# Kernel tuning notes

Measured on AMD Instinct MI355X. Metric: run time of the kernel, lower is better.

Reference implementation:

```python
import jax, jax.numpy as jnp
import numpy as np

COMMITMENT_COST = 0.25


def setup_inputs() -> dict:
    key = jax.random.key(0)
    k1, k2 = jax.random.split(key)
    inputs = jax.random.normal(k1, (16, 4096, 256), dtype=jnp.float32)
    codewords = jax.random.normal(k2, (1024, 256), dtype=jnp.float32)
    return {"inputs": inputs, "codewords": codewords}


def reference(inputs, codewords):
    # inputs: (*, D), codewords: (K, D)
    D = codewords.shape[-1]
    flat = inputs.reshape(-1, D)  # (N, D)
    x_sq = jnp.sum(flat * flat, axis=-1, keepdims=True)            # (N, 1)
    c_sq = jnp.sum(codewords * codewords, axis=-1)                 # (K,)
    distances = x_sq - 2.0 * (flat @ codewords.T) + c_sq           # (N, K)
    encoding_indices = jnp.argmin(distances, axis=1)               # (N,)
    quantized = codewords[encoding_indices].reshape(inputs.shape)  # (*, D)
    # Straight-through estimator
    quantized_st = inputs + jax.lax.stop_gradient(quantized - inputs)
    quantizing_loss = jnp.mean((quantized_st - jax.lax.stop_gradient(inputs)) ** 2)
    commitment_loss = jnp.mean((jax.lax.stop_gradient(quantized_st) - inputs) ** 2)
    loss = quantizing_loss + COMMITMENT_COST * commitment_loss
    return quantized_st, encoding_indices.reshape(inputs.shape[:-1]), loss
```

## Files before the change

kernel.cpp:

```cpp
#include <hip/hip_runtime.h>
#include <math.h>

typedef _Float16 v8h __attribute__((ext_vector_type(8)));
typedef float v4f __attribute__((ext_vector_type(4)));

constexpr int D      = 256;
constexpr int KS     = 8;
constexpr int TILE_B = 8192;
constexpr int TPW    = 2;
constexpr int WIN_B  = 16384;
constexpr int NWIN   = 32;
#define GUARD 1.0f

__global__ void vq_prep(const float* __restrict__ cw, unsigned short* __restrict__ img) {
    int gid = blockIdx.x * 256 + threadIdx.x;
    int t  = gid >> 9;
    int r  = gid & 511;
    int ks = r >> 6;
    int l  = r & 63;
    int cand = t * 16 + (l & 15);
    int k0   = ks * 32 + (l >> 4) * 8;
    const float* src = cw + (size_t)cand * D + k0;
    float4 t0 = *(const float4*)(src);
    float4 t1 = *(const float4*)(src + 4);
    v8h h;
    h[0] = (_Float16)t0.x; h[1] = (_Float16)t0.y;
    h[2] = (_Float16)t0.z; h[3] = (_Float16)t0.w;
    h[4] = (_Float16)t1.x; h[5] = (_Float16)t1.y;
    h[6] = (_Float16)t1.z; h[7] = (_Float16)t1.w;
    *(v8h*)((char*)img + (size_t)gid * 16) = h;
}

__global__ void vq_csq(const float* __restrict__ cw, float* __restrict__ csq) {
    int k = blockIdx.x * blockDim.x + threadIdx.x;
    const float4* p = reinterpret_cast<const float4*>(cw + (size_t)k * D);
    float s = 0.f;
    #pragma unroll 8
    for (int i = 0; i < D / 4; ++i) {
        float4 v = p[i];
        s += v.x * v.x; s += v.y * v.y; s += v.z * v.z; s += v.w * v.w;
    }
    csq[k] = s;
}

__launch_bounds__(256, 2)
__global__ void vq_main(const float* __restrict__ inp,
                        const float* __restrict__ cw,
                        const unsigned short* __restrict__ img,
                        const float* __restrict__ csq,
                        float* __restrict__ outq,
                        float* __restrict__ outi,
                        float* __restrict__ bsum) {
    __shared__ __align__(16) char smem[3][WIN_B];
    __shared__ float s_cq[1024];
    __shared__ int4  s_pack[128];
    __shared__ float s_xsq[128];
    __shared__ int   s_win[128];
    __shared__ float s_l[4];

    const int tid  = threadIdx.x;
    const int lane = tid & 63;
    const int w    = tid >> 6;
    const int lr   = lane & 15;
    const int q    = lane >> 4;
    const int base = blockIdx.x * 128 + w * 32;

#define VQ_STAGE(WIN, BUF)                                                           \
    {                                                                                \
        const char* srct = (const char*)img + (size_t)(WIN) * WIN_B;                 \
        _Pragma("unroll")                                                            \
        for (int i = 0; i < 4; ++i) {                                                \
            int off = i * 4096 + w * 1024;                                           \
            __builtin_amdgcn_global_load_lds(                                        \
                (const __attribute__((address_space(1))) unsigned int*)(srct + off + lane * 16), \
                (__attribute__((address_space(3))) unsigned int*)(&smem[BUF][off]),  \
                16, 0, 0);                                                           \
        }                                                                            \
    }

    VQ_STAGE(0, 0)
    VQ_STAGE(1, 1)

    {
        float4 cv4 = ((const float4*)csq)[tid];
        s_cq[tid * 4 + 0] = cv4.x + 4096.f;
        s_cq[tid * 4 + 1] = cv4.y + 4096.f;
        s_cq[tid * 4 + 2] = cv4.z + 4096.f;
        s_cq[tid * 4 + 3] = cv4.w + 4096.f;
    }

    v8h a2[2][8];
    #pragma unroll
    for (int m = 0; m < 2; ++m) {
        const float* rp = inp + (size_t)(base + m * 16 + lr) * D + q * 8;
        float sq = 0.f;
        #pragma unroll
        for (int ks = 0; ks < KS; ++ks) {
            float4 t0 = *(const float4*)(rp + ks * 32);
            float4 t1 = *(const float4*)(rp + ks * 32 + 4);
            sq = fmaf(t0.x, t0.x, sq); sq = fmaf(t0.y, t0.y, sq);
            sq = fmaf(t0.z, t0.z, sq); sq = fmaf(t0.w, t0.w, sq);
            sq = fmaf(t1.x, t1.x, sq); sq = fmaf(t1.y, t1.y, sq);
            sq = fmaf(t1.z, t1.z, sq); sq = fmaf(t1.w, t1.w, sq);
            v8h h;
            h[0] = (_Float16)(-2.f * t0.x); h[1] = (_Float16)(-2.f * t0.y);
            h[2] = (_Float16)(-2.f * t0.z); h[3] = (_Float16)(-2.f * t0.w);
            h[4] = (_Float16)(-2.f * t1.x); h[5] = (_Float16)(-2.f * t1.y);
            h[6] = (_Float16)(-2.f * t1.z); h[7] = (_Float16)(-2.f * t1.w);
            a2[m][ks] = h;
        }
        sq += __shfl_xor(sq, 16);
        sq += __shfl_xor(sq, 32);
        if (q == 0) s_xsq[w * 32 + m * 16 + lr] = sq;
    }

    const float BIGF = __uint_as_float(0x7F000000u);
    float v1[2][4], v2[2][4];
    #pragma unroll
    for (int m = 0; m < 2; ++m)
        #pragma unroll
        for (int r = 0; r < 4; ++r) { v1[m][r] = BIGF; v2[m][r] = BIGF; }

    __syncthreads();

#define VQ_COMPUTE(BUF, WIN)                                                         \
    {                                                                                \
        float cq0 = s_cq[(2 * (WIN)) * 16 + lr];                                     \
        float cq1 = s_cq[(2 * (WIN) + 1) * 16 + lr];                                 \
        v4f a00 = {cq0, cq0, cq0, cq0}; v4f a01 = a00;                               \
        v4f a10 = {cq1, cq1, cq1, cq1}; v4f a11 = a10;                               \
        const char* bb = smem[BUF];                                                  \
        __builtin_amdgcn_s_setprio(1);                                               \
        _Pragma("unroll")                                                            \
        for (int ks = 0; ks < KS; ++ks) {                                            \
            v8h b0 = *(const v8h*)(bb + ks * 1024 + lane * 16);                      \
            v8h b1 = *(const v8h*)(bb + TILE_B + ks * 1024 + lane * 16);             \
            a00 = __builtin_amdgcn_mfma_f32_16x16x32_f16(a2[0][ks], b0, a00, 0, 0, 0); \
            a10 = __builtin_amdgcn_mfma_f32_16x16x32_f16(a2[0][ks], b1, a10, 0, 0, 0); \
            a01 = __builtin_amdgcn_mfma_f32_16x16x32_f16(a2[1][ks], b0, a01, 0, 0, 0); \
            a11 = __builtin_amdgcn_mfma_f32_16x16x32_f16(a2[1][ks], b1, a11, 0, 0, 0); \
        }                                                                            \
        __builtin_amdgcn_s_setprio(0);                                               \
        unsigned idx0 = (unsigned)((2 * (WIN)) * 16) | (unsigned)lr;                 \
        unsigned idx1 = (unsigned)((2 * (WIN) + 1) * 16) | (unsigned)lr;             \
        _Pragma("unroll")                                                            \
        for (int r = 0; r < 4; ++r) {                                                \
            float f;                                                                 \
            f = __uint_as_float(((__float_as_uint(a00[r]) + 0x200u) & 0xFFFFFC00u) | idx0); \
            { float mx = fmaxf(v1[0][r], f); v2[0][r] = fminf(v2[0][r], mx); v1[0][r] = fminf(v1[0][r], f); } \
            f = __uint_as_float(((__float_as_uint(a01[r]) + 0x200u) & 0xFFFFFC00u) | idx0); \
            { float mx = fmaxf(v1[1][r], f); v2[1][r] = fminf(v2[1][r], mx); v1[1][r] = fminf(v1[1][r], f); } \
            f = __uint_as_float(((__float_as_uint(a10[r]) + 0x200u) & 0xFFFFFC00u) | idx1); \
            { float mx = fmaxf(v1[0][r], f); v2[0][r] = fminf(v2[0][r], mx); v1[0][r] = fminf(v1[0][r], f); } \
            f = __uint_as_float(((__float_as_uint(a11[r]) + 0x200u) & 0xFFFFFC00u) | idx1); \
            { float mx = fmaxf(v1[1][r], f); v2[1][r] = fminf(v2[1][r], mx); v1[1][r] = fminf(v1[1][r], f); } \
        }                                                                            \
    }

    int cm = 0;
    int st = 2;
    for (int win = 0; win < NWIN - 1; ++win) {
        asm volatile("s_waitcnt vmcnt(4)" ::: "memory");
        __builtin_amdgcn_s_barrier();
        __builtin_amdgcn_sched_barrier(0);
        if (win + 2 < NWIN) VQ_STAGE(win + 2, st)
        __builtin_amdgcn_sched_barrier(0);
        VQ_COMPUTE(cm, win)
        cm = (cm == 2) ? 0 : cm + 1;
        st = (st == 2) ? 0 : st + 1;
    }
    asm volatile("s_waitcnt vmcnt(0)" ::: "memory");
    __builtin_amdgcn_s_barrier();
    __builtin_amdgcn_sched_barrier(0);
    VQ_COMPUTE(cm, NWIN - 1)
#undef VQ_COMPUTE
#undef VQ_STAGE

    #pragma unroll
    for (int m = 0; m < 2; ++m)
        #pragma unroll
        for (int r = 0; r < 4; ++r) {
            float L0 = v1[m][r], L1 = v2[m][r], L2 = BIGF, L3 = BIGF;
            #pragma unroll
            for (int off = 8; off; off >>= 1) {
                float P0 = __shfl_xor(L0, off, 16);
                float P1 = __shfl_xor(L1, off, 16);
                float P2 = __shfl_xor(L2, off, 16);
                float P3 = __shfl_xor(L3, off, 16);
                float M0 = fminf(L0, P3), M1 = fminf(L1, P2);
                float M2 = fminf(L2, P1), M3 = fminf(L3, P0);
                float a0 = fminf(M0, M2), c0 = fmaxf(M0, M2);
                float b0 = fminf(M1, M3), d0 = fmaxf(M1, M3);
                L0 = fminf(a0, b0); L1 = fmaxf(a0, b0);
                L2 = fminf(c0, d0); L3 = fmaxf(c0, d0);
            }
            if (lr == 0) {
                int rloc = m * 16 + q * 4 + r;
                s_pack[w * 32 + rloc] = make_int4(
                    (int)__float_as_uint(L0), (int)__float_as_uint(L1),
                    (int)__float_as_uint(L2), (int)__float_as_uint(L3));
            }
        }

    const int c = lane & 3;
    float lacc = 0.f;
    #pragma unroll
    for (int h = 0; h < 2; ++h) {
        int rloc = h * 16 + (lane >> 2);
        int grow = base + rloc;
        int4 pk = s_pack[w * 32 + rloc];
        float L0 = __uint_as_float((unsigned)pk.x);
        float L1 = __uint_as_float((unsigned)pk.y);
        float L2 = __uint_as_float((unsigned)pk.z);
        float L3 = __uint_as_float((unsigned)pk.w);
        float xq = s_xsq[w * 32 + rloc];

        int   bi;
        float bd;
        bool rescue = (L1 - L0) < GUARD;
        if (rescue) {
            float Lc = (c == 0) ? L0 : (c == 1) ? L1 : (c == 2) ? L2 : L3;
            int cd = (int)(__float_as_uint(Lc) & 1023u);
            const float4* xp = (const float4*)(inp + (size_t)grow * D);
            const float4* cp = (const float4*)(cw + (size_t)cd * D);
            float dot = 0.f, xsq = 0.f;
            #pragma unroll 8
            for (int i = 0; i < D / 4; ++i) {
                float4 xv = xp[i];
                float4 cv = cp[i];
                xsq = fmaf(xv.x, xv.x, xsq);
                xsq = fmaf(xv.y, xv.y, xsq);
                xsq = fmaf(xv.z, xv.z, xsq);
                xsq = fmaf(xv.w, xv.w, xsq);
                dot = fmaf(xv.x, cv.x, dot);
                dot = fmaf(xv.y, cv.y, dot);
                dot = fmaf(xv.z, cv.z, dot);
                dot = fmaf(xv.w, cv.w, dot);
            }
            float m2 = dot + dot;
            float t  = xsq - m2;
            float e  = t + csq[cd];
            bd = e; bi = cd;
            #pragma unroll
            for (int off = 1; off <= 2; off <<= 1) {
                float ev = __shfl_xor(bd, off, 4);
                int   iv = __shfl_xor(bi, off, 4);
                bool  tk = (ev < bd) || (ev == bd && iv < bi);
                bd = tk ? ev : bd;
                bi = tk ? iv : bi;
            }
        } else {
            bi = (int)(__float_as_uint(L0) & 1023u);
            bd = (L0 - 4096.f) + xq;
        }

        if (c == 0) { s_win[w * 32 + rloc] = bi; lacc += bd; }
    }

    #pragma unroll 4
    for (int rr = 0; rr < 32; ++rr) {
        int bw = s_win[w * 32 + rr];
        float4 cv = *(const float4*)(cw + (size_t)bw * D + lane * 4);
        *(float4*)(outq + (size_t)(base + rr) * D + lane * 4) = cv;
        if (lane == 0) outi[base + rr] = (float)bw;
    }

    #pragma unroll
    for (int off = 32; off; off >>= 1) lacc += __shfl_xor(lacc, off);
    if (lane == 0) s_l[w] = lacc;
    __syncthreads();
    if (tid == 0) bsum[blockIdx.x] = s_l[0] + s_l[1] + s_l[2] + s_l[3];
}

__global__ void vq_finalize(const float* __restrict__ bsum, float* __restrict__ out_loss,
                            int nb, float scale) {
    __shared__ float s[4];
    int tid = threadIdx.x;
    float v = 0.f;
    for (int i = tid; i < nb; i += 256) v += bsum[i];
    #pragma unroll
    for (int off = 32; off; off >>= 1) v += __shfl_down(v, off, 64);
    if ((tid & 63) == 0) s[tid >> 6] = v;
    __syncthreads();
    if (tid == 0) out_loss[0] = (s[0] + s[1] + s[2] + s[3]) * scale;
}

extern "C" void kernel_launch(void* const* d_in, const int* in_sizes, int n_in,
                              void* d_out, int out_size, void* d_ws, size_t ws_size,
                              hipStream_t stream) {
    const float* inp = (const float*)d_in[0];
    const float* cw  = (const float*)d_in[1];
    float* out = (float*)d_out;
    const int N = in_sizes[0] / D;
    const int K = in_sizes[1] / D;

    char* ws = (char*)d_ws;
    unsigned short* img = (unsigned short*)ws;
    float* csq  = (float*)(ws + (size_t)K * D * 2);
    float* bsum = csq + K;

    float* outq = out;
    float* outi = out + (size_t)N * D;
    float* outl = outi + N;

    vq_prep<<<dim3((K * 32) / 256), dim3(256), 0, stream>>>(cw, img);
    vq_csq<<<dim3(K / 256), dim3(256), 0, stream>>>(cw, csq);

    vq_main<<<dim3(N / 128), dim3(256), 0, stream>>>(inp, cw, img, csq,
                                                     outq, outi, bsum);
    vq_finalize<<<dim3(1), dim3(256), 0, stream>>>(bsum, outl, N / 128,
                                                   1.25f / ((float)N * (float)D));
}
```

Measured before the change: 91.10 us.

## Split codeword windows across wave pairs with 64 rows per wave

Waves are paired: each wave now holds 64 input rows (four 16-row A fragments) and computes only half of each staged codeword window, so each wave reads one B fragment per k-step and reuses it across four MFMAs instead of two. The codeword image layout is permuted in the prep kernel so each window's two halves are contiguous, and per-row top-4 candidates from the two halves are merged through shared memory after an added block barrier. This cuts LDS reads per MFMA but doubles the A-fragment registers per wave, which may reduce occupancy, and duplicates the input-row loads across wave pairs.

```diff
diff --git a/kernel.cpp b/kernel.cpp
--- a/kernel.cpp
+++ b/kernel.cpp
@@ -6,8 +6,7 @@
 
 constexpr int D      = 256;
 constexpr int KS     = 8;
-constexpr int TILE_B = 8192;
-constexpr int TPW    = 2;
+constexpr int HALF_B = 8192;
 constexpr int WIN_B  = 16384;
 constexpr int NWIN   = 32;
 #define GUARD 1.0f
@@ -28,7 +27,8 @@
     h[2] = (_Float16)t0.z; h[3] = (_Float16)t0.w;
     h[4] = (_Float16)t1.x; h[5] = (_Float16)t1.y;
     h[6] = (_Float16)t1.z; h[7] = (_Float16)t1.w;
-    *(v8h*)((char*)img + (size_t)gid * 16) = h;
+    size_t dst = (size_t)(t & 31) * WIN_B + (size_t)(t >> 5) * HALF_B + ks * 1024 + l * 16;
+    *(v8h*)((char*)img + dst) = h;
 }
 
 __global__ void vq_csq(const float* __restrict__ cw, float* __restrict__ csq) {
@@ -53,7 +53,7 @@
                         float* __restrict__ bsum) {
     __shared__ __align__(16) char smem[3][WIN_B];
     __shared__ float s_cq[1024];
-    __shared__ int4  s_pack[128];
+    __shared__ int4  s_pk[2][128];
     __shared__ float s_xsq[128];
     __shared__ int   s_win[128];
     __shared__ float s_l[4];
@@ -61,9 +61,11 @@
     const int tid  = threadIdx.x;
     const int lane = tid & 63;
     const int w    = tid >> 6;
+    const int hh   = w & 1;
+    const int g    = w >> 1;
     const int lr   = lane & 15;
     const int q    = lane >> 4;
-    const int base = blockIdx.x * 128 + w * 32;
+    const int rbase = blockIdx.x * 128 + g * 64;
 
 #define VQ_STAGE(WIN, BUF)                                                           \
     {                                                                                \
@@ -89,10 +91,10 @@
         s_cq[tid * 4 + 3] = cv4.w + 4096.f;
     }
 
-    v8h a2[2][8];
-    #pragma unroll
-    for (int m = 0; m < 2; ++m) {
-        const float* rp = inp + (size_t)(base + m * 16 + lr) * D + q * 8;
+    v8h a2[4][8];
+    #pragma unroll
+    for (int m = 0; m < 4; ++m) {
+        const float* rp = inp + (size_t)(rbase + m * 16 + lr) * D + q * 8;
         float sq = 0.f;
         #pragma unroll
         for (int ks = 0; ks < KS; ++ks) {
@@ -111,13 +113,13 @@
         }
         sq += __shfl_xor(sq, 16);
         sq += __shfl_xor(sq, 32);
-        if (q == 0) s_xsq[w * 32 + m * 16 + lr] = sq;
+        if (hh == 0 && q == 0) s_xsq[g * 64 + m * 16 + lr] = sq;
     }
 
     const float BIGF = __uint_as_float(0x7F000000u);
-    float v1[2][4], v2[2][4];
-    #pragma unroll
-    for (int m = 0; m < 2; ++m)
+    float v1[4][4], v2[4][4];
+    #pragma unroll
+    for (int m = 0; m < 4; ++m)
         #pragma unroll
         for (int r = 0; r < 4; ++r) { v1[m][r] = BIGF; v2[m][r] = BIGF; }
 
@@ -125,40 +127,36 @@
 
 #define VQ_COMPUTE(BUF, WIN)                                                         \
     {                                                                                \
-        float cq0 = s_cq[(2 * (WIN)) * 16 + lr];                                     \
-        float cq1 = s_cq[(2 * (WIN) + 1) * 16 + lr];                                 \
-        v4f a00 = {cq0, cq0, cq0, cq0}; v4f a01 = a00;                               \
-        v4f a10 = {cq1, cq1, cq1, cq1}; v4f a11 = a10;                               \
-        const char* bb = smem[BUF];                                                  \
+        const int tile = (WIN) + (hh << 5);                                          \
+        float cq = s_cq[tile * 16 + lr];                                             \
+        v4f a0 = {cq, cq, cq, cq}; v4f a1 = a0; v4f aa2 = a0; v4f a3 = a0;           \
+        const char* bb = smem[BUF] + hh * HALF_B;                                    \
         __builtin_amdgcn_s_setprio(1);                                               \
         _Pragma("unroll")                                                            \
         for (int ks = 0; ks < KS; ++ks) {                                            \
-            v8h b0 = *(const v8h*)(bb + ks * 1024 + lane * 16);                      \
-            v8h b1 = *(const v8h*)(bb + TILE_B + ks * 1024 + lane * 16);             \
-            a00 = __builtin_amdgcn_mfma_f32_16x16x32_f16(a2[0][ks], b0, a00, 0, 0, 0); \
-            a10 = __builtin_amdgcn_mfma_f32_16x16x32_f16(a2[0][ks], b1, a10, 0, 0, 0); \
-            a01 = __builtin_amdgcn_mfma_f32_16x16x32_f16(a2[1][ks], b0, a01, 0, 0, 0); \
-            a11 = __builtin_amdgcn_mfma_f32_16x16x32_f16(a2[1][ks], b1, a11, 0, 0, 0); \
+            v8h b = *(const v8h*)(bb + ks * 1024 + lane * 16);                       \
+            a0  = __builtin_amdgcn_mfma_f32_16x16x32_f16(a2[0][ks], b, a0,  0, 0, 0); \
+            a1  = __builtin_amdgcn_mfma_f32_16x16x32_f16(a2[1][ks], b, a1,  0, 0, 0); \
+            aa2 = __builtin_amdgcn_mfma_f32_16x16x32_f16(a2[2][ks], b, aa2, 0, 0, 0); \
+            a3  = __builtin_amdgcn_mfma_f32_16x16x32_f16(a2[3][ks], b, a3,  0, 0, 0); \
         }                                                                            \
         __builtin_amdgcn_s_setprio(0);                                               \
-        unsigned idx0 = (unsigned)((2 * (WIN)) * 16) | (unsigned)lr;                 \
-        unsigned idx1 = (unsigned)((2 * (WIN) + 1) * 16) | (unsigned)lr;             \
+        unsigned idx = (unsigned)(tile * 16) | (unsigned)lr;                         \
         _Pragma("unroll")                                                            \
         for (int r = 0; r < 4; ++r) {                                                \
             float f;                                                                 \
-            f = __uint_as_float(((__float_as_uint(a00[r]) + 0x200u) & 0xFFFFFC00u) | idx0); \
+            f = __uint_as_float(((__float_as_uint(a0[r])  + 0x200u) & 0xFFFFFC00u) | idx); \
             { float mx = fmaxf(v1[0][r], f); v2[0][r] = fminf(v2[0][r], mx); v1[0][r] = fminf(v1[0][r], f); } \
-            f = __uint_as_float(((__float_as_uint(a01[r]) + 0x200u) & 0xFFFFFC00u) | idx0); \
+            f = __uint_as_float(((__float_as_uint(a1[r])  + 0x200u) & 0xFFFFFC00u) | idx); \
             { float mx = fmaxf(v1[1][r], f); v2[1][r] = fminf(v2[1][r], mx); v1[1][r] = fminf(v1[1][r], f); } \
-            f = __uint_as_float(((__float_as_uint(a10[r]) + 0x200u) & 0xFFFFFC00u) | idx1); \
-            { float mx = fmaxf(v1[0][r], f); v2[0][r] = fminf(v2[0][r], mx); v1[0][r] = fminf(v1[0][r], f); } \
-            f = __uint_as_float(((__float_as_uint(a11[r]) + 0x200u) & 0xFFFFFC00u) | idx1); \
-            { float mx = fmaxf(v1[1][r], f); v2[1][r] = fminf(v2[1][r], mx); v1[1][r] = fminf(v1[1][r], f); } \
+            f = __uint_as_float(((__float_as_uint(aa2[r]) + 0x200u) & 0xFFFFFC00u) | idx); \
+            { float mx = fmaxf(v1[2][r], f); v2[2][r] = fminf(v2[2][r], mx); v1[2][r] = fminf(v1[2][r], f); } \
+            f = __uint_as_float(((__float_as_uint(a3[r])  + 0x200u) & 0xFFFFFC00u) | idx); \
+            { float mx = fmaxf(v1[3][r], f); v2[3][r] = fminf(v2[3][r], mx); v1[3][r] = fminf(v1[3][r], f); } \
         }                                                                            \
     }
 
-    int cm = 0;
-    int st = 2;
+    int cm = 0, st = 2;
     for (int win = 0; win < NWIN - 1; ++win) {
         asm volatile("s_waitcnt vmcnt(4)" ::: "memory");
         __builtin_amdgcn_s_barrier();
@@ -177,7 +175,7 @@
 #undef VQ_STAGE
 
     #pragma unroll
-    for (int m = 0; m < 2; ++m)
+    for (int m = 0; m < 4; ++m)
         #pragma unroll
         for (int r = 0; r < 4; ++r) {
             float L0 = v1[m][r], L1 = v2[m][r], L2 = BIGF, L3 = BIGF;
@@ -195,25 +193,34 @@
                 L2 = fminf(c0, d0); L3 = fmaxf(c0, d0);
             }
             if (lr == 0) {
-                int rloc = m * 16 + q * 4 + r;
-                s_pack[w * 32 + rloc] = make_int4(
+                int row = g * 64 + m * 16 + q * 4 + r;
+                s_pk[hh][row] = make_int4(
                     (int)__float_as_uint(L0), (int)__float_as_uint(L1),
                     (int)__float_as_uint(L2), (int)__float_as_uint(L3));
             }
         }
-
-    const int c = lane & 3;
+    __syncthreads();
+
+    const int c  = lane & 3;
+    const int eb = blockIdx.x * 128 + w * 32;
     float lacc = 0.f;
     #pragma unroll
-    for (int h = 0; h < 2; ++h) {
-        int rloc = h * 16 + (lane >> 2);
-        int grow = base + rloc;
-        int4 pk = s_pack[w * 32 + rloc];
-        float L0 = __uint_as_float((unsigned)pk.x);
-        float L1 = __uint_as_float((unsigned)pk.y);
-        float L2 = __uint_as_float((unsigned)pk.z);
-        float L3 = __uint_as_float((unsigned)pk.w);
-        float xq = s_xsq[w * 32 + rloc];
+    for (int h2 = 0; h2 < 2; ++h2) {
+        int rloc = h2 * 16 + (lane >> 2);
+        int brow = w * 32 + rloc;
+        int grow = eb + rloc;
+        int4 pa = s_pk[0][brow];
+        int4 pb = s_pk[1][brow];
+        float a0 = __uint_as_float((unsigned)pa.x), a1 = __uint_as_float((unsigned)pa.y);
+        float a2f = __uint_as_float((unsigned)pa.z), a3 = __uint_as_float((unsigned)pa.w);
+        float b0 = __uint_as_float((unsigned)pb.x), b1 = __uint_as_float((unsigned)pb.y);
+        float b2 = __uint_as_float((unsigned)pb.z), b3 = __uint_as_float((unsigned)pb.w);
+        float M0 = fminf(a0, b3), M1 = fminf(a1, b2), M2 = fminf(a2f, b1), M3 = fminf(a3, b0);
+        float t0 = fminf(M0, M2), t2 = fmaxf(M0, M2);
+        float t1 = fminf(M1, M3), t3 = fmaxf(M1, M3);
+        float L0 = fminf(t0, t1), L1 = fmaxf(t0, t1);
+        float L2 = fminf(t2, t3), L3 = fmaxf(t2, t3);
+        float xq = s_xsq[brow];
 
         int   bi;
         float bd;
@@ -254,15 +261,15 @@
             bd = (L0 - 4096.f) + xq;
         }
 
-        if (c == 0) { s_win[w * 32 + rloc] = bi; lacc += bd; }
+        if (c == 0) { s_win[brow] = bi; lacc += bd; }
     }
 
     #pragma unroll 4
     for (int rr = 0; rr < 32; ++rr) {
         int bw = s_win[w * 32 + rr];
         float4 cv = *(const float4*)(cw + (size_t)bw * D + lane * 4);
-        *(float4*)(outq + (size_t)(base + rr) * D + lane * 4) = cv;
-        if (lane == 0) outi[base + rr] = (float)bw;
+        *(float4*)(outq + (size_t)(eb + rr) * D + lane * 4) = cv;
+        if (lane == 0) outi[eb + rr] = (float)bw;
     }
 
     #pragma unroll
```

Measured after the change: 105.3 us. 1.16x slower.
